# Performance work log

Measured on AMD Instinct MI355X. Metric: run time of the kernel, lower is better.

The kernel has to match this reference:

```python
import jax, jax.numpy as jnp
import numpy as np

ROT_DELTA = 1  # rotation_delta from __init__
BN_EPS = 1e-3  # keras BatchNormalization default epsilon


def conv_dirac(signal, bc_idx, bc_w, W, b):
    """Template-based intrinsic mesh conv (dirac patch operator).

    signal: [N, D]; bc_idx/bc_w: [N, Rr, A, 3]; W: [T, Rr, A, D]; b: [T].
    Returns [N, K, T] with K = A // ROT_DELTA rotations.
    """
    gathered = signal[bc_idx]  # [N, Rr, A, 3, D] irregular gather
    interp = jnp.einsum('vrai,vraid->vrad', bc_w, gathered)  # barycentric interp
    A = interp.shape[2]
    rots = np.arange(0, A, ROT_DELTA)
    # Rotating the (small) template weights is equivalent to rolling the
    # interpolated signal along the angular axis, but far cheaper.
    W_rot = jnp.stack([jnp.roll(W, int(r), axis=2) for r in rots])  # [K, T, Rr, A, D]
    return jnp.einsum('vrad,ktrad->vkt', interp, W_rot) + b  # [N, K, T]


def angular_max_pool(x):
    # Select, per vertex, the rotation whose response has maximal L2 norm.
    k = jnp.argmax(jnp.linalg.norm(x, axis=-1), axis=1)  # [N]
    return jnp.take_along_axis(x, k[:, None, None], axis=1)[:, 0]  # [N, T]


def batch_norm(x, gamma, beta):
    mu = jnp.mean(x, axis=0, keepdims=True)
    var = jnp.var(x, axis=0, keepdims=True)
    return gamma * (x - mu) * jax.lax.rsqrt(var + BN_EPS) + beta


def setup_inputs() -> dict:
    key = jax.random.key(0)
    ks = jax.random.split(key, 6)
    N, Rr, A, D, T = 80000, 5, 8, 32, 32
    signal = jax.random.normal(ks[0], (N, D), dtype=jnp.float32)
    bc_idx = jax.random.randint(ks[1], (N, Rr, A, 3), 0, N)
    bc_w = jax.random.uniform(ks[2], (N, Rr, A, 3), dtype=jnp.float32)
    bc_w = bc_w / jnp.sum(bc_w, axis=-1, keepdims=True)  # barycentric coords sum to 1
    W1 = jax.random.normal(ks[3], (T, Rr, A, D), dtype=jnp.float32) * 0.05
    W2 = jax.random.normal(ks[4], (T, Rr, A, D), dtype=jnp.float32) * 0.05
    return {
        'signal': signal, 'bc_idx': bc_idx, 'bc_w': bc_w,
        'W1': W1, 'b1': jnp.zeros((T,), jnp.float32),
        'gamma1': jnp.ones((T,), jnp.float32), 'beta1': jnp.zeros((T,), jnp.float32),
        'W2': W2, 'b2': jnp.zeros((T,), jnp.float32),
        'gamma2': jnp.ones((T,), jnp.float32), 'beta2': jnp.zeros((T,), jnp.float32),
    }


def reference(signal, bc_idx, bc_w, W1, b1, gamma1, beta1, W2, b2, gamma2, beta2):
    # Branch 1: conv -> angular max-pool -> BN -> relu
    s = conv_dirac(signal, bc_idx, bc_w, W1, b1)
    s = angular_max_pool(s)
    s = batch_norm(s, gamma1, beta1)
    s = jax.nn.relu(s)
    # Branch 2: conv -> angular max-pool -> BN
    s = conv_dirac(s, bc_idx, bc_w, W2, b2)
    s = angular_max_pool(s)
    s = batch_norm(s, gamma2, beta2)
    # Residual add (input_dim == amt_templates -> no rescale branch) + activation
    return jax.nn.relu(s + signal)
```

## Files before the change

### kernel.cpp

```cpp
#include <hip/hip_runtime.h>
#include <math.h>

#define RR 5
#define AA 8
#define DD 32
#define TT 32
#define KK 8

#define RT2 0.70710678118654752f

typedef float v2f __attribute__((ext_vector_type(2)));
typedef float v4f __attribute__((ext_vector_type(4)));

static __device__ __forceinline__ v2f pkfma(v2f a, v2f b, v2f c) {
#if __has_builtin(__builtin_elementwise_fma)
    return __builtin_elementwise_fma(a, b, c);
#else
    v2f r; r.x = fmaf(a.x, b.x, c.x); r.y = fmaf(a.y, b.y, c.y); return r;
#endif
}

__global__ void wdft_kernel(const float* __restrict__ W, float* __restrict__ Ws) {
    int idx = blockIdx.x * 256 + threadIdx.x;
    if (idx >= TT * RR * DD) return;
    int d = idx & 31;
    int tr = idx >> 5;
    int t = tr / 5;
    int r = tr - t * 5;
    float xa[8];
    #pragma unroll
    for (int a = 0; a < 8; ++a) xa[a] = W[(tr * 8 + a) * 32 + d];
    float s0 = xa[0] + xa[4], d0 = xa[0] - xa[4];
    float s1 = xa[1] + xa[5], d1 = xa[1] - xa[5];
    float s2 = xa[2] + xa[6], d2 = xa[2] - xa[6];
    float s3 = xa[3] + xa[7], d3 = xa[3] - xa[7];
    float s02 = s0 + s2, s13 = s1 + s3;
    float F0 = s02 + s13, F4 = s02 - s13;
    float R2 = s0 - s2, I2 = s3 - s1;
    float u = RT2 * (d1 - d3), v = RT2 * (d1 + d3);
    float R1 = d0 + u, R3 = d0 - u;
    float I1 = -d2 - v, I3 = d2 - v;
    float* o = &Ws[(size_t)(((r * 32 + d) * 32 + t) * 8)];
    o[0] = F0; o[1] = F4; o[2] = R1; o[3] = I1;
    o[4] = R2; o[5] = I2; o[6] = R3; o[7] = I3;
}

__global__ __launch_bounds__(256, 2)
void fused_conv_kernel(const float* __restrict__ sig,
                       const int* __restrict__ bc_idx,
                       const float* __restrict__ bc_w,
                       const float* __restrict__ Wsg,
                       const float* __restrict__ bias,
                       float* __restrict__ s_out,
                       int N) {
    __shared__ float Is[64 * 260];
    __shared__ float Wl[8 * 260];

    int tid = threadIdx.x;
    int vBase = blockIdx.x * 64;
    int lane = tid & 63;
    int wv = tid >> 6;

    int vg = lane & 7;
    int tg = lane >> 3;
    int v0L = wv * 16 + vg * 2;
    int v0 = vBase + v0L;
    int v1 = v0 + 1;

    int d2 = tid & 15;
    int g = tid >> 4;

    v2f A0[2][4], A1[2][4], A2[2][4], A3[2][4];
    #pragma unroll
    for (int vv = 0; vv < 2; ++vv)
        #pragma unroll
        for (int j = 0; j < 4; ++j) {
            A0[vv][j] = (v2f){0.f, 0.f}; A1[vv][j] = (v2f){0.f, 0.f};
            A2[vv][j] = (v2f){0.f, 0.f}; A3[vv][j] = (v2f){0.f, 0.f};
        }

    const v2f rt2 = {RT2, RT2};
    const v4f* Ws4 = (const v4f*)Wsg;

    for (int r = 0; r < RR; ++r) {
        __syncthreads();

        #pragma unroll
        for (int vv0 = 0; vv0 < 4; ++vv0) {
            int vv = g + vv0 * 16;
            int vgl = vBase + vv;
            int vgc = (vgl < N) ? vgl : (N - 1);
            int base = (vgc * 40 + r * 8) * 3;
            v2f xa[8];
            #pragma unroll
            for (int a = 0; a < 8; ++a) {
                int i0 = bc_idx[base + a * 3 + 0];
                int i1 = bc_idx[base + a * 3 + 1];
                int i2 = bc_idx[base + a * 3 + 2];
                float w0 = bc_w[base + a * 3 + 0];
                float w1 = bc_w[base + a * 3 + 1];
                float w2 = bc_w[base + a * 3 + 2];
                v2f r0 = *(const v2f*)&sig[(size_t)i0 * 32 + 2 * d2];
                v2f r1 = *(const v2f*)&sig[(size_t)i1 * 32 + 2 * d2];
                v2f r2 = *(const v2f*)&sig[(size_t)i2 * 32 + 2 * d2];
                v2f w0v = {w0, w0};
                v2f w1v = {w1, w1};
                v2f w2v = {w2, w2};
                xa[a] = pkfma(w2v, r2, pkfma(w1v, r1, w0v * r0));
            }
            v2f s0 = xa[0] + xa[4], dd0 = xa[0] - xa[4];
            v2f s1 = xa[1] + xa[5], dd1 = xa[1] - xa[5];
            v2f s2 = xa[2] + xa[6], dd2 = xa[2] - xa[6];
            v2f s3 = xa[3] + xa[7], dd3 = xa[3] - xa[7];
            v2f s02 = s0 + s2, s13 = s1 + s3;
            v2f F0 = s02 + s13, F4 = s02 - s13;
            v2f R2 = s0 - s2, I2 = s3 - s1;
            v2f u = rt2 * (dd1 - dd3), vvv = rt2 * (dd1 + dd3);
            v2f R1 = dd0 + u, R3 = dd0 - u;
            v2f I1 = -dd2 - vvv, I3 = dd2 - vvv;
            float* ob = &Is[vv * 260 + (2 * d2) * 8];
            *(v4f*)&ob[0]  = (v4f){F0.x, F4.x, R1.x, I1.x};
            *(v4f*)&ob[4]  = (v4f){R2.x, I2.x, R3.x, I3.x};
            *(v4f*)&ob[8]  = (v4f){F0.y, F4.y, R1.y, I1.y};
            *(v4f*)&ob[12] = (v4f){R2.y, I2.y, R3.y, I3.y};
        }

        for (int ws = 0; ws < 4; ++ws) {
            __syncthreads();
            {
                const v4f* src = Ws4 + (size_t)(r * 32 + ws * 8) * 64;
                int dl = tid >> 5;
                int rem = (tid * 8) & 255;
                float* dst = &Wl[dl * 260 + rem];
                v4f a = src[tid * 2];
                v4f b = src[tid * 2 + 1];
                *(v4f*)dst = a;
                *(v4f*)(dst + 4) = b;
            }
            __syncthreads();

            #pragma unroll 2
            for (int dl = 0; dl < 8; ++dl) {
                int dg = ws * 8 + dl;
                const float* ip = &Is[v0L * 260 + dg * 8];
                v4f pa0 = *(const v4f*)&ip[0];
                v4f pb0 = *(const v4f*)&ip[4];
                v4f pa1 = *(const v4f*)&ip[260];
                v4f pb1 = *(const v4f*)&ip[264];
                v2f x1_0 = pa0.zw, x1n_0 = {pa0.w, -pa0.z};
                v2f x2_0 = pb0.xy, x2n_0 = {pb0.y, -pb0.x};
                v2f x3_0 = pb0.zw, x3n_0 = {pb0.w, -pb0.z};
                v2f x1_1 = pa1.zw, x1n_1 = {pa1.w, -pa1.z};
                v2f x2_1 = pb1.xy, x2n_1 = {pb1.y, -pb1.x};
                v2f x3_1 = pb1.zw, x3n_1 = {pb1.w, -pb1.z};
                const float* wrow = &Wl[dl * 260];
                #pragma unroll
                for (int j = 0; j < 4; ++j) {
                    v4f q0 = *(const v4f*)&wrow[(tg + 8 * j) * 8];
                    v4f q1 = *(const v4f*)&wrow[(tg + 8 * j) * 8 + 4];
                    v2f w2v = {q0.z, q0.z}, w3v = {q0.w, q0.w};
                    v2f w4v = {q1.x, q1.x}, w5v = {q1.y, q1.y};
                    v2f w6v = {q1.z, q1.z}, w7v = {q1.w, q1.w};
                    A0[0][j] = pkfma(pa0.xy, q0.xy, A0[0][j]);
                    A1[0][j] = pkfma(x1_0, w2v, A1[0][j]);
                    A1[0][j] = pkfma(x1n_0, w3v, A1[0][j]);
                    A2[0][j] = pkfma(x2_0, w4v, A2[0][j]);
                    A2[0][j] = pkfma(x2n_0, w5v, A2[0][j]);
                    A3[0][j] = pkfma(x3_0, w6v, A3[0][j]);
                    A3[0][j] = pkfma(x3n_0, w7v, A3[0][j]);
                    A0[1][j] = pkfma(pa1.xy, q0.xy, A0[1][j]);
                    A1[1][j] = pkfma(x1_1, w2v, A1[1][j]);
                    A1[1][j] = pkfma(x1n_1, w3v, A1[1][j]);
                    A2[1][j] = pkfma(x2_1, w4v, A2[1][j]);
                    A2[1][j] = pkfma(x2n_1, w5v, A2[1][j]);
                    A3[1][j] = pkfma(x3_1, w6v, A3[1][j]);
                    A3[1][j] = pkfma(x3n_1, w7v, A3[1][j]);
                }
            }
        }
    }

    float bj[4];
    #pragma unroll
    for (int j = 0; j < 4; ++j) bj[j] = bias[tg + 8 * j];

    float outk[2][8][4];
    #pragma unroll
    for (int vv = 0; vv < 2; ++vv) {
        #pragma unroll
        for (int j = 0; j < 4; ++j) {
            float C0 = A0[vv][j].x, C4 = A0[vv][j].y;
            float R1 = A1[vv][j].x, I1 = A1[vv][j].y;
            float R2 = A2[vv][j].x, I2 = A2[vv][j].y;
            float R3 = A3[vv][j].x, I3 = A3[vv][j].y;
            float e = 0.125f * (C0 + C4), o = 0.125f * (C0 - C4);
            float p = 0.25f * (R1 + R3), q = 0.25f * R2, s = 0.25f * (I1 - I3);
            float a_ = 0.25f * RT2 * (R1 - R3);
            float b_ = 0.25f * RT2 * (I1 + I3);
            float c_ = 0.25f * I2;
            float bb = bj[j];
            outk[vv][0][j] = e + p + q + bb;
            outk[vv][1][j] = o + a_ - b_ - c_ + bb;
            outk[vv][2][j] = e - s - q + bb;
            outk[vv][3][j] = o - a_ - b_ + c_ + bb;
            outk[vv][4][j] = e - p + q + bb;
            outk[vv][5][j] = o - a_ + b_ - c_ + bb;
            outk[vv][6][j] = e + s - q + bb;
            outk[vv][7][j] = o + a_ + b_ + c_ + bb;
        }
    }

    #pragma unroll
    for (int vv = 0; vv < 2; ++vv) {
        float norms[8];
        #pragma unroll
        for (int k = 0; k < 8; ++k) {
            float nl = 0.f;
            #pragma unroll
            for (int j = 0; j < 4; ++j)
                nl = fmaf(outk[vv][k][j], outk[vv][k][j], nl);
            nl += __shfl_xor(nl, 8);
            nl += __shfl_xor(nl, 16);
            nl += __shfl_xor(nl, 32);
            norms[k] = nl;
        }
        float best = -1.f;
        int bk = 0;
        #pragma unroll
        for (int k = 0; k < 8; ++k) {
            float n = sqrtf(norms[k]);
            if (n > best) { best = n; bk = k; }
        }
        int vOut = (vv == 0) ? v0 : v1;
        if (vOut < N) {
            float sel[4];
            #pragma unroll
            for (int j = 0; j < 4; ++j) sel[j] = 0.f;
            #pragma unroll
            for (int k = 0; k < 8; ++k) {
                if (k == bk) {
                    #pragma unroll
                    for (int j = 0; j < 4; ++j) sel[j] = outk[vv][k][j];
                }
            }
            float* o = s_out + (size_t)vOut * 32 + tg;
            o[0]  = sel[0];
            o[8]  = sel[1];
            o[16] = sel[2];
            o[24] = sel[3];
        }
    }
}

__global__ void stats_kernel(const float* __restrict__ s,
                             double* __restrict__ sums,
                             double* __restrict__ sumsq, int n) {
    __shared__ double la[256];
    __shared__ double lb[256];
    int tid = threadIdx.x;
    int t = tid & 31;
    int row = tid >> 5;
    double a = 0.0, b = 0.0;
    for (int v = blockIdx.x * 8 + row; v < n; v += gridDim.x * 8) {
        float x = s[(size_t)v * 32 + t];
        a += (double)x;
        b += (double)x * (double)x;
    }
    la[tid] = a; lb[tid] = b;
    __syncthreads();
    for (int off = 128; off >= 32; off >>= 1) {
        if (tid < off) { la[tid] += la[tid + off]; lb[tid] += lb[tid + off]; }
        __syncthreads();
    }
    if (tid < 32) {
        atomicAdd(&sums[t], la[tid]);
        atomicAdd(&sumsq[t], lb[tid]);
    }
}

__global__ void finalize_kernel(const double* __restrict__ sums,
                                const double* __restrict__ sumsq,
                                const float* __restrict__ gamma,
                                const float* __restrict__ beta,
                                float* __restrict__ scale,
                                float* __restrict__ shift, int n) {
    int t = threadIdx.x;
    if (t < 32) {
        double mu = sums[t] / (double)n;
        double var = sumsq[t] / (double)n - mu * mu;
        double sc = (double)gamma[t] / sqrt(var + 1e-3);
        scale[t] = (float)sc;
        shift[t] = (float)((double)beta[t] - mu * sc);
    }
}

__global__ void affine_relu_kernel(const float* __restrict__ s,
                                   const float* __restrict__ scale,
                                   const float* __restrict__ shift,
                                   float* __restrict__ o, int n4) {
    int e = blockIdx.x * blockDim.x + threadIdx.x;
    if (e >= n4) return;
    int t0 = (e & 7) * 4;
    float4 x = ((const float4*)s)[e];
    float4 y;
    y.x = fmaxf(fmaf(scale[t0 + 0], x.x, shift[t0 + 0]), 0.f);
    y.y = fmaxf(fmaf(scale[t0 + 1], x.y, shift[t0 + 1]), 0.f);
    y.z = fmaxf(fmaf(scale[t0 + 2], x.z, shift[t0 + 2]), 0.f);
    y.w = fmaxf(fmaf(scale[t0 + 3], x.w, shift[t0 + 3]), 0.f);
    ((float4*)o)[e] = y;
}

__global__ void final_kernel(const float* __restrict__ s,
                             const float* __restrict__ scale,
                             const float* __restrict__ shift,
                             const float* __restrict__ sig,
                             float* __restrict__ o, int n4) {
    int e = blockIdx.x * blockDim.x + threadIdx.x;
    if (e >= n4) return;
    int t0 = (e & 7) * 4;
    float4 x = ((const float4*)s)[e];
    float4 z = ((const float4*)sig)[e];
    float4 y;
    y.x = fmaxf(fmaf(scale[t0 + 0], x.x, shift[t0 + 0]) + z.x, 0.f);
    y.y = fmaxf(fmaf(scale[t0 + 1], x.y, shift[t0 + 1]) + z.y, 0.f);
    y.z = fmaxf(fmaf(scale[t0 + 2], x.z, shift[t0 + 2]) + z.z, 0.f);
    y.w = fmaxf(fmaf(scale[t0 + 3], x.w, shift[t0 + 3]) + z.w, 0.f);
    ((float4*)o)[e] = y;
}

__global__ void zero_stats_kernel(double* __restrict__ d, float* __restrict__ f) {
    int t = threadIdx.x;
    if (t < 128) d[t] = 0.0;
    if (t < 128) f[t] = 0.f;
}

extern "C" void kernel_launch(void* const* d_in, const int* in_sizes, int n_in,
                              void* d_out, int out_size, void* d_ws, size_t ws_size,
                              hipStream_t stream) {
    const float* signal = (const float*)d_in[0];
    const int* bc_idx   = (const int*)d_in[1];
    const float* bc_w   = (const float*)d_in[2];
    const float* W1     = (const float*)d_in[3];
    const float* b1     = (const float*)d_in[4];
    const float* g1     = (const float*)d_in[5];
    const float* be1    = (const float*)d_in[6];
    const float* W2     = (const float*)d_in[7];
    const float* b2     = (const float*)d_in[8];
    const float* g2     = (const float*)d_in[9];
    const float* be2    = (const float*)d_in[10];
    float* out = (float*)d_out;

    const int N = in_sizes[0] / 32;

    char* ws = (char*)d_ws;
    double* sums1  = (double*)ws;
    double* sumsq1 = sums1 + 32;
    double* sums2  = sums1 + 64;
    double* sumsq2 = sums1 + 96;
    float* scale1 = (float*)(ws + 1024);
    float* shift1 = scale1 + 32;
    float* scale2 = scale1 + 64;
    float* shift2 = scale1 + 96;
    float* Ws1 = (float*)(ws + 4096);
    float* Ws2 = Ws1 + RR * DD * TT * 8;
    float* s1  = Ws2 + RR * DD * TT * 8;
    float* sg2 = s1 + (size_t)N * 32;
    float* s2  = sg2 + (size_t)N * 32;

    int nBlocks = (N + 63) / 64;
    int wBlocks = (TT * RR * DD + 255) / 256;

    zero_stats_kernel<<<1, 128, 0, stream>>>((double*)ws, (float*)(ws + 1024));
    wdft_kernel<<<wBlocks, 256, 0, stream>>>(W1, Ws1);
    wdft_kernel<<<wBlocks, 256, 0, stream>>>(W2, Ws2);

    fused_conv_kernel<<<nBlocks, 256, 0, stream>>>(signal, bc_idx, bc_w, Ws1, b1, s1, N);
    stats_kernel<<<64, 256, 0, stream>>>(s1, sums1, sumsq1, N);
    finalize_kernel<<<1, 32, 0, stream>>>(sums1, sumsq1, g1, be1, scale1, shift1, N);
    affine_relu_kernel<<<(N * 8 + 255) / 256, 256, 0, stream>>>(s1, scale1, shift1, sg2, N * 8);

    fused_conv_kernel<<<nBlocks, 256, 0, stream>>>(sg2, bc_idx, bc_w, Ws2, b2, s2, N);
    stats_kernel<<<64, 256, 0, stream>>>(s2, sums2, sumsq2, N);
    finalize_kernel<<<1, 32, 0, stream>>>(sums2, sumsq2, g2, be2, scale2, shift2, N);

    final_kernel<<<(N * 8 + 255) / 256, 256, 0, stream>>>(s2, scale2, shift2, signal, out, N * 8);
}
```

Baseline: 714.8 us.

## Tile conv kernel over 128 vertices with half-D staging and 4 vertices per thread

The fused conv kernel now processes 128 vertices per block. The D dimension is split into two halves of 16, and each thread gathers float4 signal chunks. Each thread accumulates 4 vertices instead of 2, so every weight value read from LDS is reused across more vertices, and the interpolation staging buffer shrinks per half. The weight DFT is also relaid out to match the new LDS layout. The costs are more accumulator registers, which may reduce occupancy, and more block syncs per radial step.

Result: slower. 2.426 ms (+239.3%).

```diff
diff --git a/kernel.cpp b/kernel.cpp
--- a/kernel.cpp
+++ b/kernel.cpp
@@ -17,6 +17,14 @@
     return __builtin_elementwise_fma(a, b, c);
 #else
     v2f r; r.x = fmaf(a.x, b.x, c.x); r.y = fmaf(a.y, b.y, c.y); return r;
+#endif
+}
+static __device__ __forceinline__ v4f pkfma4(v4f a, v4f b, v4f c) {
+#if __has_builtin(__builtin_elementwise_fma)
+    return __builtin_elementwise_fma(a, b, c);
+#else
+    v4f r; r.x = fmaf(a.x, b.x, c.x); r.y = fmaf(a.y, b.y, c.y);
+    r.z = fmaf(a.z, b.z, c.z); r.w = fmaf(a.w, b.w, c.w); return r;
 #endif
 }
 
@@ -40,9 +48,13 @@
     float u = RT2 * (d1 - d3), v = RT2 * (d1 + d3);
     float R1 = d0 + u, R3 = d0 - u;
     float I1 = -d2 - v, I3 = d2 - v;
-    float* o = &Ws[(size_t)(((r * 32 + d) * 32 + t) * 8)];
-    o[0] = F0; o[1] = F4; o[2] = R1; o[3] = I1;
-    o[4] = R2; o[5] = I2; o[6] = R3; o[7] = I3;
+    int h = d >> 4;
+    int sub = (d >> 3) & 1;
+    int dl = d & 7;
+    float* o0 = &Ws[(size_t)(((r * 2 + h) * 2 + sub) * 2 + 0) * 1024 + dl * 128 + t * 4];
+    float* o1 = o0 + 1024;
+    o0[0] = F0; o0[1] = F4; o0[2] = R1; o0[3] = I1;
+    o1[0] = R2; o1[1] = I2; o1[2] = R3; o1[3] = I3;
 }
 
 __global__ __launch_bounds__(256, 2)
@@ -53,128 +65,130 @@
                        const float* __restrict__ bias,
                        float* __restrict__ s_out,
                        int N) {
-    __shared__ float Is[64 * 260];
-    __shared__ float Wl[8 * 260];
+    __shared__ float Is[128 * 132];
+    __shared__ float Wl[2048];
 
     int tid = threadIdx.x;
-    int vBase = blockIdx.x * 64;
+    int vBase = blockIdx.x * 128;
     int lane = tid & 63;
     int wv = tid >> 6;
 
     int vg = lane & 7;
     int tg = lane >> 3;
-    int v0L = wv * 16 + vg * 2;
-    int v0 = vBase + v0L;
-    int v1 = v0 + 1;
-
-    int d2 = tid & 15;
-    int g = tid >> 4;
-
-    v2f A0[2][4], A1[2][4], A2[2][4], A3[2][4];
+
+    int d4 = tid & 3;
+    int g = tid >> 2;
+
+    v2f A0[4][4], A1[4][4], A2[4][4], A3[4][4];
     #pragma unroll
-    for (int vv = 0; vv < 2; ++vv)
+    for (int vv = 0; vv < 4; ++vv)
         #pragma unroll
         for (int j = 0; j < 4; ++j) {
             A0[vv][j] = (v2f){0.f, 0.f}; A1[vv][j] = (v2f){0.f, 0.f};
             A2[vv][j] = (v2f){0.f, 0.f}; A3[vv][j] = (v2f){0.f, 0.f};
         }
 
-    const v2f rt2 = {RT2, RT2};
-    const v4f* Ws4 = (const v4f*)Wsg;
-
     for (int r = 0; r < RR; ++r) {
-        __syncthreads();
-
-        #pragma unroll
-        for (int vv0 = 0; vv0 < 4; ++vv0) {
-            int vv = g + vv0 * 16;
-            int vgl = vBase + vv;
-            int vgc = (vgl < N) ? vgl : (N - 1);
-            int base = (vgc * 40 + r * 8) * 3;
-            v2f xa[8];
-            #pragma unroll
-            for (int a = 0; a < 8; ++a) {
-                int i0 = bc_idx[base + a * 3 + 0];
-                int i1 = bc_idx[base + a * 3 + 1];
-                int i2 = bc_idx[base + a * 3 + 2];
-                float w0 = bc_w[base + a * 3 + 0];
-                float w1 = bc_w[base + a * 3 + 1];
-                float w2 = bc_w[base + a * 3 + 2];
-                v2f r0 = *(const v2f*)&sig[(size_t)i0 * 32 + 2 * d2];
-                v2f r1 = *(const v2f*)&sig[(size_t)i1 * 32 + 2 * d2];
-                v2f r2 = *(const v2f*)&sig[(size_t)i2 * 32 + 2 * d2];
-                v2f w0v = {w0, w0};
-                v2f w1v = {w1, w1};
-                v2f w2v = {w2, w2};
-                xa[a] = pkfma(w2v, r2, pkfma(w1v, r1, w0v * r0));
+        for (int h = 0; h < 2; ++h) {
+            __syncthreads();
+
+            {
+                const float* src = Wsg + (size_t)((r * 2 + h) * 2 + 0) * 2048 + tid * 8;
+                v4f a = *(const v4f*)src;
+                v4f b = *(const v4f*)(src + 4);
+                *(v4f*)&Wl[tid * 8] = a;
+                *(v4f*)&Wl[tid * 8 + 4] = b;
             }
-            v2f s0 = xa[0] + xa[4], dd0 = xa[0] - xa[4];
-            v2f s1 = xa[1] + xa[5], dd1 = xa[1] - xa[5];
-            v2f s2 = xa[2] + xa[6], dd2 = xa[2] - xa[6];
-            v2f s3 = xa[3] + xa[7], dd3 = xa[3] - xa[7];
-            v2f s02 = s0 + s2, s13 = s1 + s3;
-            v2f F0 = s02 + s13, F4 = s02 - s13;
-            v2f R2 = s0 - s2, I2 = s3 - s1;
-            v2f u = rt2 * (dd1 - dd3), vvv = rt2 * (dd1 + dd3);
-            v2f R1 = dd0 + u, R3 = dd0 - u;
-            v2f I1 = -dd2 - vvv, I3 = dd2 - vvv;
-            float* ob = &Is[vv * 260 + (2 * d2) * 8];
-            *(v4f*)&ob[0]  = (v4f){F0.x, F4.x, R1.x, I1.x};
-            *(v4f*)&ob[4]  = (v4f){R2.x, I2.x, R3.x, I3.x};
-            *(v4f*)&ob[8]  = (v4f){F0.y, F4.y, R1.y, I1.y};
-            *(v4f*)&ob[12] = (v4f){R2.y, I2.y, R3.y, I3.y};
-        }
-
-        for (int ws = 0; ws < 4; ++ws) {
-            __syncthreads();
-            {
-                const v4f* src = Ws4 + (size_t)(r * 32 + ws * 8) * 64;
-                int dl = tid >> 5;
-                int rem = (tid * 8) & 255;
-                float* dst = &Wl[dl * 260 + rem];
-                v4f a = src[tid * 2];
-                v4f b = src[tid * 2 + 1];
-                *(v4f*)dst = a;
-                *(v4f*)(dst + 4) = b;
+
+            #pragma unroll
+            for (int pass = 0; pass < 2; ++pass) {
+                int vv = g + 64 * pass;
+                int vgl = vBase + vv;
+                int vgc = (vgl < N) ? vgl : (N - 1);
+                int base = (vgc * 40 + r * 8) * 3;
+                v4f xa[8];
+                #pragma unroll
+                for (int a = 0; a < 8; ++a) {
+                    int i0 = bc_idx[base + a * 3 + 0];
+                    int i1 = bc_idx[base + a * 3 + 1];
+                    int i2 = bc_idx[base + a * 3 + 2];
+                    float w0 = bc_w[base + a * 3 + 0];
+                    float w1 = bc_w[base + a * 3 + 1];
+                    float w2 = bc_w[base + a * 3 + 2];
+                    v4f r0 = *(const v4f*)&sig[(size_t)i0 * 32 + h * 16 + d4 * 4];
+                    v4f r1 = *(const v4f*)&sig[(size_t)i1 * 32 + h * 16 + d4 * 4];
+                    v4f r2 = *(const v4f*)&sig[(size_t)i2 * 32 + h * 16 + d4 * 4];
+                    v4f w0v = {w0, w0, w0, w0};
+                    v4f w1v = {w1, w1, w1, w1};
+                    v4f w2v = {w2, w2, w2, w2};
+                    xa[a] = pkfma4(w2v, r2, pkfma4(w1v, r1, w0v * r0));
+                }
+                v4f s0 = xa[0] + xa[4], dd0 = xa[0] - xa[4];
+                v4f s1 = xa[1] + xa[5], dd1 = xa[1] - xa[5];
+                v4f s2 = xa[2] + xa[6], dd2 = xa[2] - xa[6];
+                v4f s3 = xa[3] + xa[7], dd3 = xa[3] - xa[7];
+                v4f s02 = s0 + s2, s13 = s1 + s3;
+                v4f F0 = s02 + s13, F4 = s02 - s13;
+                v4f R2 = s0 - s2, I2 = s3 - s1;
+                v4f rt2v = {RT2, RT2, RT2, RT2};
+                v4f u = rt2v * (dd1 - dd3), vvv = rt2v * (dd1 + dd3);
+                v4f R1 = dd0 + u, R3 = dd0 - u;
+                v4f I1 = -dd2 - vvv, I3 = dd2 - vvv;
+                float* ob = &Is[vv * 132];
+                #pragma unroll
+                for (int c = 0; c < 4; ++c) {
+                    int dloc = 4 * d4 + c;
+                    *(v4f*)&ob[dloc * 4]      = (v4f){F0[c], F4[c], R1[c], I1[c]};
+                    *(v4f*)&ob[64 + dloc * 4] = (v4f){R2[c], I2[c], R3[c], I3[c]};
+                }
             }
-            __syncthreads();
-
-            #pragma unroll 2
-            for (int dl = 0; dl < 8; ++dl) {
-                int dg = ws * 8 + dl;
-                const float* ip = &Is[v0L * 260 + dg * 8];
-                v4f pa0 = *(const v4f*)&ip[0];
-                v4f pb0 = *(const v4f*)&ip[4];
-                v4f pa1 = *(const v4f*)&ip[260];
-                v4f pb1 = *(const v4f*)&ip[264];
-                v2f x1_0 = pa0.zw, x1n_0 = {pa0.w, -pa0.z};
-                v2f x2_0 = pb0.xy, x2n_0 = {pb0.y, -pb0.x};
-                v2f x3_0 = pb0.zw, x3n_0 = {pb0.w, -pb0.z};
-                v2f x1_1 = pa1.zw, x1n_1 = {pa1.w, -pa1.z};
-                v2f x2_1 = pb1.xy, x2n_1 = {pb1.y, -pb1.x};
-                v2f x3_1 = pb1.zw, x3n_1 = {pb1.w, -pb1.z};
-                const float* wrow = &Wl[dl * 260];
-                #pragma unroll
-                for (int j = 0; j < 4; ++j) {
-                    v4f q0 = *(const v4f*)&wrow[(tg + 8 * j) * 8];
-                    v4f q1 = *(const v4f*)&wrow[(tg + 8 * j) * 8 + 4];
-                    v2f w2v = {q0.z, q0.z}, w3v = {q0.w, q0.w};
-                    v2f w4v = {q1.x, q1.x}, w5v = {q1.y, q1.y};
-                    v2f w6v = {q1.z, q1.z}, w7v = {q1.w, q1.w};
-                    A0[0][j] = pkfma(pa0.xy, q0.xy, A0[0][j]);
-                    A1[0][j] = pkfma(x1_0, w2v, A1[0][j]);
-                    A1[0][j] = pkfma(x1n_0, w3v, A1[0][j]);
-                    A2[0][j] = pkfma(x2_0, w4v, A2[0][j]);
-                    A2[0][j] = pkfma(x2n_0, w5v, A2[0][j]);
-                    A3[0][j] = pkfma(x3_0, w6v, A3[0][j]);
-                    A3[0][j] = pkfma(x3n_0, w7v, A3[0][j]);
-                    A0[1][j] = pkfma(pa1.xy, q0.xy, A0[1][j]);
-                    A1[1][j] = pkfma(x1_1, w2v, A1[1][j]);
-                    A1[1][j] = pkfma(x1n_1, w3v, A1[1][j]);
-                    A2[1][j] = pkfma(x2_1, w4v, A2[1][j]);
-                    A2[1][j] = pkfma(x2n_1, w5v, A2[1][j]);
-                    A3[1][j] = pkfma(x3_1, w6v, A3[1][j]);
-                    A3[1][j] = pkfma(x3n_1, w7v, A3[1][j]);
+
+            #pragma unroll
+            for (int sub = 0; sub < 2; ++sub) {
+                if (sub == 1) {
+                    __syncthreads();
+                    const float* src = Wsg + (size_t)((r * 2 + h) * 2 + 1) * 2048 + tid * 8;
+                    v4f a = *(const v4f*)src;
+                    v4f b = *(const v4f*)(src + 4);
+                    *(v4f*)&Wl[tid * 8] = a;
+                    *(v4f*)&Wl[tid * 8 + 4] = b;
+                }
+                __syncthreads();
+
+                #pragma unroll 2
+                for (int dl = 0; dl < 8; ++dl) {
+                    int dloc = sub * 8 + dl;
+                    v4f p0[4], p1[4];
+                    #pragma unroll
+                    for (int vv = 0; vv < 4; ++vv) {
+                        int vrow = wv * 32 + vg + vv * 8;
+                        p0[vv] = *(const v4f*)&Is[vrow * 132 + dloc * 4];
+                        p1[vv] = *(const v4f*)&Is[vrow * 132 + 64 + dloc * 4];
+                    }
+                    #pragma unroll
+                    for (int j = 0; j < 4; ++j) {
+                        v4f q0 = *(const v4f*)&Wl[dl * 128 + (tg + 8 * j) * 4];
+                        v4f q1 = *(const v4f*)&Wl[1024 + dl * 128 + (tg + 8 * j) * 4];
+                        v2f w2v = {q0.z, q0.z}, w3v = {q0.w, q0.w};
+                        v2f w4v = {q1.x, q1.x}, w5v = {q1.y, q1.y};
+                        v2f w6v = {q1.z, q1.z}, w7v = {q1.w, q1.w};
+                        #pragma unroll
+                        for (int vv = 0; vv < 4; ++vv) {
+                            v2f x1 = p0[vv].zw;
+                            v2f x1n = {p0[vv].w, -p0[vv].z};
+                            v2f x2 = p1[vv].xy;
+                            v2f x2n = {p1[vv].y, -p1[vv].x};
+                            v2f x3 = p1[vv].zw;
+                            v2f x3n = {p1[vv].w, -p1[vv].z};
+                            A0[vv][j] = pkfma(p0[vv].xy, q0.xy, A0[vv][j]);
+                            A1[vv][j] = pkfma(x1, w2v, A1[vv][j]);
+                            A1[vv][j] = pkfma(x1n, w3v, A1[vv][j]);
+                            A2[vv][j] = pkfma(x2, w4v, A2[vv][j]);
+                            A2[vv][j] = pkfma(x2n, w5v, A2[vv][j]);
+                            A3[vv][j] = pkfma(x3, w6v, A3[vv][j]);
+                            A3[vv][j] = pkfma(x3n, w7v, A3[vv][j]);
+                        }
+                    }
                 }
             }
         }
@@ -184,9 +198,9 @@
     #pragma unroll
     for (int j = 0; j < 4; ++j) bj[j] = bias[tg + 8 * j];
 
-    float outk[2][8][4];
     #pragma unroll
-    for (int vv = 0; vv < 2; ++vv) {
+    for (int vv = 0; vv < 4; ++vv) {
+        float outk[8][4];
         #pragma unroll
         for (int j = 0; j < 4; ++j) {
             float C0 = A0[vv][j].x, C4 = A0[vv][j].y;
@@ -199,26 +213,22 @@
             float b_ = 0.25f * RT2 * (I1 + I3);
             float c_ = 0.25f * I2;
             float bb = bj[j];
-            outk[vv][0][j] = e + p + q + bb;
-            outk[vv][1][j] = o + a_ - b_ - c_ + bb;
-            outk[vv][2][j] = e - s - q + bb;
-            outk[vv][3][j] = o - a_ - b_ + c_ + bb;
-            outk[vv][4][j] = e - p + q + bb;
-            outk[vv][5][j] = o - a_ + b_ - c_ + bb;
-            outk[vv][6][j] = e + s - q + bb;
-            outk[vv][7][j] = o + a_ + b_ + c_ + bb;
-        }
-    }
-
-    #pragma unroll
-    for (int vv = 0; vv < 2; ++vv) {
+            outk[0][j] = e + p + q + bb;
+            outk[1][j] = o + a_ - b_ - c_ + bb;
+            outk[2][j] = e - s - q + bb;
+            outk[3][j] = o - a_ - b_ + c_ + bb;
+            outk[4][j] = e - p + q + bb;
+            outk[5][j] = o - a_ + b_ - c_ + bb;
+            outk[6][j] = e + s - q + bb;
+            outk[7][j] = o + a_ + b_ + c_ + bb;
+        }
         float norms[8];
         #pragma unroll
         for (int k = 0; k < 8; ++k) {
             float nl = 0.f;
             #pragma unroll
             for (int j = 0; j < 4; ++j)
-                nl = fmaf(outk[vv][k][j], outk[vv][k][j], nl);
+                nl = fmaf(outk[k][j], outk[k][j], nl);
             nl += __shfl_xor(nl, 8);
             nl += __shfl_xor(nl, 16);
             nl += __shfl_xor(nl, 32);
@@ -231,7 +241,7 @@
             float n = sqrtf(norms[k]);
             if (n > best) { best = n; bk = k; }
         }
-        int vOut = (vv == 0) ? v0 : v1;
+        int vOut = vBase + wv * 32 + vg + vv * 8;
         if (vOut < N) {
             float sel[4];
             #pragma unroll
@@ -240,7 +250,7 @@
             for (int k = 0; k < 8; ++k) {
                 if (k == bk) {
                     #pragma unroll
-                    for (int j = 0; j < 4; ++j) sel[j] = outk[vv][k][j];
+                    for (int j = 0; j < 4; ++j) sel[j] = outk[k][j];
                 }
             }
             float* o = s_out + (size_t)vOut * 32 + tg;
@@ -367,7 +377,7 @@
     float* sg2 = s1 + (size_t)N * 32;
     float* s2  = sg2 + (size_t)N * 32;
 
-    int nBlocks = (N + 63) / 64;
+    int nBlocks = (N + 127) / 128;
     int wBlocks = (TT * RR * DD + 255) / 256;
 
     zero_stats_kernel<<<1, 128, 0, stream>>>((double*)ws, (float*)(ws + 1024));
```

## Fuse BN1+ReLU into second conv gather and halve shared-memory tiles for occupancy

Applied to the files above, without the earlier changes.

Removes the standalone affine+ReLU pass by applying BN1 scale/shift and ReLU to gathered neighbor values inside the second conv kernel, which is templated on an AFFINE flag. The conv now processes the feature dimension in two halves of 16, with a new weight layout and a smaller shared-memory footprint. This allows launch bounds of 3 blocks per SM. Each gathered value is now re-transformed per use (three neighbors per angle), and the interpolation stage syncs more often, trading extra ALU work and barriers for one fewer full-tensor read/write and higher occupancy.

After: 808.7 us. 13.1% more time.

```diff
diff --git a/kernel.cpp b/kernel.cpp
--- a/kernel.cpp
+++ b/kernel.cpp
@@ -40,21 +40,27 @@
     float u = RT2 * (d1 - d3), v = RT2 * (d1 + d3);
     float R1 = d0 + u, R3 = d0 - u;
     float I1 = -d2 - v, I3 = d2 - v;
-    float* o = &Ws[(size_t)(((r * 32 + d) * 32 + t) * 8)];
-    o[0] = F0; o[1] = F4; o[2] = R1; o[3] = I1;
-    o[4] = R2; o[5] = I2; o[6] = R3; o[7] = I3;
-}
-
-__global__ __launch_bounds__(256, 2)
+    int h = d >> 4;
+    int dl = d & 15;
+    float* o0 = &Ws[(size_t)(r * 2 + h) * 4096 + dl * 128 + t * 4];
+    float* o1 = o0 + 2048;
+    o0[0] = F0; o0[1] = F4; o0[2] = R1; o0[3] = I1;
+    o1[0] = R2; o1[1] = I2; o1[2] = R3; o1[3] = I3;
+}
+
+template <bool AFFINE>
+__global__ __launch_bounds__(256, 3)
 void fused_conv_kernel(const float* __restrict__ sig,
                        const int* __restrict__ bc_idx,
                        const float* __restrict__ bc_w,
                        const float* __restrict__ Wsg,
                        const float* __restrict__ bias,
                        float* __restrict__ s_out,
+                       const float* __restrict__ scaleIn,
+                       const float* __restrict__ shiftIn,
                        int N) {
-    __shared__ float Is[64 * 260];
-    __shared__ float Wl[8 * 260];
+    __shared__ float Is[64 * 132];
+    __shared__ float Wl[4096];
 
     int tid = threadIdx.x;
     int vBase = blockIdx.x * 64;
@@ -63,12 +69,18 @@
 
     int vg = lane & 7;
     int tg = lane >> 3;
-    int v0L = wv * 16 + vg * 2;
-    int v0 = vBase + v0L;
-    int v1 = v0 + 1;
-
-    int d2 = tid & 15;
-    int g = tid >> 4;
+
+    int d2 = tid & 7;
+    int g = tid >> 3;
+
+    v2f scH[2], shH[2];
+    if (AFFINE) {
+        #pragma unroll
+        for (int h = 0; h < 2; ++h) {
+            scH[h] = *(const v2f*)&scaleIn[h * 16 + 2 * d2];
+            shH[h] = *(const v2f*)&shiftIn[h * 16 + 2 * d2];
+        }
+    }
 
     v2f A0[2][4], A1[2][4], A2[2][4], A3[2][4];
     #pragma unroll
@@ -80,101 +92,105 @@
         }
 
     const v2f rt2 = {RT2, RT2};
-    const v4f* Ws4 = (const v4f*)Wsg;
+    int vrow0 = (wv * 16 + vg) * 132;
+    int vrow1 = vrow0 + 8 * 132;
 
     for (int r = 0; r < RR; ++r) {
-        __syncthreads();
-
-        #pragma unroll
-        for (int vv0 = 0; vv0 < 4; ++vv0) {
-            int vv = g + vv0 * 16;
-            int vgl = vBase + vv;
-            int vgc = (vgl < N) ? vgl : (N - 1);
-            int base = (vgc * 40 + r * 8) * 3;
-            v2f xa[8];
+        #pragma unroll
+        for (int h = 0; h < 2; ++h) {
+            __syncthreads();
+
+            {
+                const v4f* src = (const v4f*)(Wsg + (size_t)(r * 2 + h) * 4096);
+                #pragma unroll
+                for (int k = 0; k < 4; ++k) {
+                    v4f val = src[k * 256 + tid];
+                    *(v4f*)&Wl[k * 1024 + tid * 4] = val;
+                }
+            }
+
             #pragma unroll
-            for (int a = 0; a < 8; ++a) {
-                int i0 = bc_idx[base + a * 3 + 0];
-                int i1 = bc_idx[base + a * 3 + 1];
-                int i2 = bc_idx[base + a * 3 + 2];
-                float w0 = bc_w[base + a * 3 + 0];
-                float w1 = bc_w[base + a * 3 + 1];
-                float w2 = bc_w[base + a * 3 + 2];
-                v2f r0 = *(const v2f*)&sig[(size_t)i0 * 32 + 2 * d2];
-                v2f r1 = *(const v2f*)&sig[(size_t)i1 * 32 + 2 * d2];
-                v2f r2 = *(const v2f*)&sig[(size_t)i2 * 32 + 2 * d2];
-                v2f w0v = {w0, w0};
-                v2f w1v = {w1, w1};
-                v2f w2v = {w2, w2};
-                xa[a] = pkfma(w2v, r2, pkfma(w1v, r1, w0v * r0));
-            }
-            v2f s0 = xa[0] + xa[4], dd0 = xa[0] - xa[4];
-            v2f s1 = xa[1] + xa[5], dd1 = xa[1] - xa[5];
-            v2f s2 = xa[2] + xa[6], dd2 = xa[2] - xa[6];
-            v2f s3 = xa[3] + xa[7], dd3 = xa[3] - xa[7];
-            v2f s02 = s0 + s2, s13 = s1 + s3;
-            v2f F0 = s02 + s13, F4 = s02 - s13;
-            v2f R2 = s0 - s2, I2 = s3 - s1;
-            v2f u = rt2 * (dd1 - dd3), vvv = rt2 * (dd1 + dd3);
-            v2f R1 = dd0 + u, R3 = dd0 - u;
-            v2f I1 = -dd2 - vvv, I3 = dd2 - vvv;
-            float* ob = &Is[vv * 260 + (2 * d2) * 8];
-            *(v4f*)&ob[0]  = (v4f){F0.x, F4.x, R1.x, I1.x};
-            *(v4f*)&ob[4]  = (v4f){R2.x, I2.x, R3.x, I3.x};
-            *(v4f*)&ob[8]  = (v4f){F0.y, F4.y, R1.y, I1.y};
-            *(v4f*)&ob[12] = (v4f){R2.y, I2.y, R3.y, I3.y};
-        }
-
-        for (int ws = 0; ws < 4; ++ws) {
-            __syncthreads();
-            {
-                const v4f* src = Ws4 + (size_t)(r * 32 + ws * 8) * 64;
-                int dl = tid >> 5;
-                int rem = (tid * 8) & 255;
-                float* dst = &Wl[dl * 260 + rem];
-                v4f a = src[tid * 2];
-                v4f b = src[tid * 2 + 1];
-                *(v4f*)dst = a;
-                *(v4f*)(dst + 4) = b;
+            for (int pass = 0; pass < 2; ++pass) {
+                int vv = g + 32 * pass;
+                int vgl = vBase + vv;
+                int vgc = (vgl < N) ? vgl : (N - 1);
+                int base = (vgc * 40 + r * 8) * 3;
+                v2f xa[8];
+                #pragma unroll
+                for (int a = 0; a < 8; ++a) {
+                    int i0 = bc_idx[base + a * 3 + 0];
+                    int i1 = bc_idx[base + a * 3 + 1];
+                    int i2 = bc_idx[base + a * 3 + 2];
+                    float w0 = bc_w[base + a * 3 + 0];
+                    float w1 = bc_w[base + a * 3 + 1];
+                    float w2 = bc_w[base + a * 3 + 2];
+                    v2f r0 = *(const v2f*)&sig[(size_t)i0 * 32 + h * 16 + 2 * d2];
+                    v2f r1 = *(const v2f*)&sig[(size_t)i1 * 32 + h * 16 + 2 * d2];
+                    v2f r2 = *(const v2f*)&sig[(size_t)i2 * 32 + h * 16 + 2 * d2];
+                    if (AFFINE) {
+                        r0.x = fmaxf(fmaf(scH[h].x, r0.x, shH[h].x), 0.f);
+                        r0.y = fmaxf(fmaf(scH[h].y, r0.y, shH[h].y), 0.f);
+                        r1.x = fmaxf(fmaf(scH[h].x, r1.x, shH[h].x), 0.f);
+                        r1.y = fmaxf(fmaf(scH[h].y, r1.y, shH[h].y), 0.f);
+                        r2.x = fmaxf(fmaf(scH[h].x, r2.x, shH[h].x), 0.f);
+                        r2.y = fmaxf(fmaf(scH[h].y, r2.y, shH[h].y), 0.f);
+                    }
+                    v2f w0v = {w0, w0};
+                    v2f w1v = {w1, w1};
+                    v2f w2v = {w2, w2};
+                    xa[a] = pkfma(w2v, r2, pkfma(w1v, r1, w0v * r0));
+                }
+                v2f s0 = xa[0] + xa[4], dd0 = xa[0] - xa[4];
+                v2f s1 = xa[1] + xa[5], dd1 = xa[1] - xa[5];
+                v2f s2 = xa[2] + xa[6], dd2 = xa[2] - xa[6];
+                v2f s3 = xa[3] + xa[7], dd3 = xa[3] - xa[7];
+                v2f s02 = s0 + s2, s13 = s1 + s3;
+                v2f F0 = s02 + s13, F4 = s02 - s13;
+                v2f R2 = s0 - s2, I2 = s3 - s1;
+                v2f u = rt2 * (dd1 - dd3), vvv = rt2 * (dd1 + dd3);
+                v2f R1 = dd0 + u, R3 = dd0 - u;
+                v2f I1 = -dd2 - vvv, I3 = dd2 - vvv;
+                float* ob = &Is[vv * 132 + d2 * 16];
+                *(v4f*)&ob[0]  = (v4f){F0.x, F4.x, R1.x, I1.x};
+                *(v4f*)&ob[4]  = (v4f){R2.x, I2.x, R3.x, I3.x};
+                *(v4f*)&ob[8]  = (v4f){F0.y, F4.y, R1.y, I1.y};
+                *(v4f*)&ob[12] = (v4f){R2.y, I2.y, R3.y, I3.y};
             }
             __syncthreads();
 
             #pragma unroll 2
-            for (int dl = 0; dl < 8; ++dl) {
-                int dg = ws * 8 + dl;
-                const float* ip = &Is[v0L * 260 + dg * 8];
-                v4f pa0 = *(const v4f*)&ip[0];
-                v4f pb0 = *(const v4f*)&ip[4];
-                v4f pa1 = *(const v4f*)&ip[260];
-                v4f pb1 = *(const v4f*)&ip[264];
-                v2f x1_0 = pa0.zw, x1n_0 = {pa0.w, -pa0.z};
-                v2f x2_0 = pb0.xy, x2n_0 = {pb0.y, -pb0.x};
-                v2f x3_0 = pb0.zw, x3n_0 = {pb0.w, -pb0.z};
-                v2f x1_1 = pa1.zw, x1n_1 = {pa1.w, -pa1.z};
-                v2f x2_1 = pb1.xy, x2n_1 = {pb1.y, -pb1.x};
-                v2f x3_1 = pb1.zw, x3n_1 = {pb1.w, -pb1.z};
-                const float* wrow = &Wl[dl * 260];
+            for (int dl = 0; dl < 16; ++dl) {
+                v4f p0a = *(const v4f*)&Is[vrow0 + dl * 8];
+                v4f p1a = *(const v4f*)&Is[vrow0 + dl * 8 + 4];
+                v4f p0b = *(const v4f*)&Is[vrow1 + dl * 8];
+                v4f p1b = *(const v4f*)&Is[vrow1 + dl * 8 + 4];
+                v2f x1a = p0a.zw, x1na = {p0a.w, -p0a.z};
+                v2f x2a = p1a.xy, x2na = {p1a.y, -p1a.x};
+                v2f x3a = p1a.zw, x3na = {p1a.w, -p1a.z};
+                v2f x1b = p0b.zw, x1nb = {p0b.w, -p0b.z};
+                v2f x2b = p1b.xy, x2nb = {p1b.y, -p1b.x};
+                v2f x3b = p1b.zw, x3nb = {p1b.w, -p1b.z};
                 #pragma unroll
                 for (int j = 0; j < 4; ++j) {
-                    v4f q0 = *(const v4f*)&wrow[(tg + 8 * j) * 8];
-                    v4f q1 = *(const v4f*)&wrow[(tg + 8 * j) * 8 + 4];
+                    v4f q0 = *(const v4f*)&Wl[dl * 128 + (tg + 8 * j) * 4];
+                    v4f q1 = *(const v4f*)&Wl[2048 + dl * 128 + (tg + 8 * j) * 4];
                     v2f w2v = {q0.z, q0.z}, w3v = {q0.w, q0.w};
                     v2f w4v = {q1.x, q1.x}, w5v = {q1.y, q1.y};
                     v2f w6v = {q1.z, q1.z}, w7v = {q1.w, q1.w};
-                    A0[0][j] = pkfma(pa0.xy, q0.xy, A0[0][j]);
-                    A1[0][j] = pkfma(x1_0, w2v, A1[0][j]);
-                    A1[0][j] = pkfma(x1n_0, w3v, A1[0][j]);
-                    A2[0][j] = pkfma(x2_0, w4v, A2[0][j]);
-                    A2[0][j] = pkfma(x2n_0, w5v, A2[0][j]);
-                    A3[0][j] = pkfma(x3_0, w6v, A3[0][j]);
-                    A3[0][j] = pkfma(x3n_0, w7v, A3[0][j]);
-                    A0[1][j] = pkfma(pa1.xy, q0.xy, A0[1][j]);
-                    A1[1][j] = pkfma(x1_1, w2v, A1[1][j]);
-                    A1[1][j] = pkfma(x1n_1, w3v, A1[1][j]);
-                    A2[1][j] = pkfma(x2_1, w4v, A2[1][j]);
-                    A2[1][j] = pkfma(x2n_1, w5v, A2[1][j]);
-                    A3[1][j] = pkfma(x3_1, w6v, A3[1][j]);
-                    A3[1][j] = pkfma(x3n_1, w7v, A3[1][j]);
+                    A0[0][j] = pkfma(p0a.xy, q0.xy, A0[0][j]);
+                    A1[0][j] = pkfma(x1a, w2v, A1[0][j]);
+                    A1[0][j] = pkfma(x1na, w3v, A1[0][j]);
+                    A2[0][j] = pkfma(x2a, w4v, A2[0][j]);
+                    A2[0][j] = pkfma(x2na, w5v, A2[0][j]);
+                    A3[0][j] = pkfma(x3a, w6v, A3[0][j]);
+                    A3[0][j] = pkfma(x3na, w7v, A3[0][j]);
+                    A0[1][j] = pkfma(p0b.xy, q0.xy, A0[1][j]);
+                    A1[1][j] = pkfma(x1b, w2v, A1[1][j]);
+                    A1[1][j] = pkfma(x1nb, w3v, A1[1][j]);
+                    A2[1][j] = pkfma(x2b, w4v, A2[1][j]);
+                    A2[1][j] = pkfma(x2nb, w5v, A2[1][j]);
+                    A3[1][j] = pkfma(x3b, w6v, A3[1][j]);
+                    A3[1][j] = pkfma(x3nb, w7v, A3[1][j]);
                 }
             }
         }
@@ -184,9 +200,9 @@
     #pragma unroll
     for (int j = 0; j < 4; ++j) bj[j] = bias[tg + 8 * j];
 
-    float outk[2][8][4];
     #pragma unroll
     for (int vv = 0; vv < 2; ++vv) {
+        float outk[8][4];
         #pragma unroll
         for (int j = 0; j < 4; ++j) {
             float C0 = A0[vv][j].x, C4 = A0[vv][j].y;
@@ -199,26 +215,22 @@
             float b_ = 0.25f * RT2 * (I1 + I3);
             float c_ = 0.25f * I2;
             float bb = bj[j];
-            outk[vv][0][j] = e + p + q + bb;
-            outk[vv][1][j] = o + a_ - b_ - c_ + bb;
-            outk[vv][2][j] = e - s - q + bb;
-            outk[vv][3][j] = o - a_ - b_ + c_ + bb;
-            outk[vv][4][j] = e - p + q + bb;
-            outk[vv][5][j] = o - a_ + b_ - c_ + bb;
-            outk[vv][6][j] = e + s - q + bb;
-            outk[vv][7][j] = o + a_ + b_ + c_ + bb;
-        }
-    }
-
-    #pragma unroll
-    for (int vv = 0; vv < 2; ++vv) {
+            outk[0][j] = e + p + q + bb;
+            outk[1][j] = o + a_ - b_ - c_ + bb;
+            outk[2][j] = e - s - q + bb;
+            outk[3][j] = o - a_ - b_ + c_ + bb;
+            outk[4][j] = e - p + q + bb;
+            outk[5][j] = o - a_ + b_ - c_ + bb;
+            outk[6][j] = e + s - q + bb;
+            outk[7][j] = o + a_ + b_ + c_ + bb;
+        }
         float norms[8];
         #pragma unroll
         for (int k = 0; k < 8; ++k) {
             float nl = 0.f;
             #pragma unroll
             for (int j = 0; j < 4; ++j)
-                nl = fmaf(outk[vv][k][j], outk[vv][k][j], nl);
+                nl = fmaf(outk[k][j], outk[k][j], nl);
             nl += __shfl_xor(nl, 8);
             nl += __shfl_xor(nl, 16);
             nl += __shfl_xor(nl, 32);
@@ -231,7 +243,7 @@
             float n = sqrtf(norms[k]);
             if (n > best) { best = n; bk = k; }
         }
-        int vOut = (vv == 0) ? v0 : v1;
+        int vOut = vBase + wv * 16 + vg + 8 * vv;
         if (vOut < N) {
             float sel[4];
             #pragma unroll
@@ -240,7 +252,7 @@
             for (int k = 0; k < 8; ++k) {
                 if (k == bk) {
                     #pragma unroll
-                    for (int j = 0; j < 4; ++j) sel[j] = outk[vv][k][j];
+                    for (int j = 0; j < 4; ++j) sel[j] = outk[k][j];
                 }
             }
             float* o = s_out + (size_t)vOut * 32 + tg;
@@ -292,22 +304,6 @@
         scale[t] = (float)sc;
         shift[t] = (float)((double)beta[t] - mu * sc);
     }
-}
-
-__global__ void affine_relu_kernel(const float* __restrict__ s,
-                                   const float* __restrict__ scale,
-                                   const float* __restrict__ shift,
-                                   float* __restrict__ o, int n4) {
-    int e = blockIdx.x * blockDim.x + threadIdx.x;
-    if (e >= n4) return;
-    int t0 = (e & 7) * 4;
-    float4 x = ((const float4*)s)[e];
-    float4 y;
-    y.x = fmaxf(fmaf(scale[t0 + 0], x.x, shift[t0 + 0]), 0.f);
-    y.y = fmaxf(fmaf(scale[t0 + 1], x.y, shift[t0 + 1]), 0.f);
-    y.z = fmaxf(fmaf(scale[t0 + 2], x.z, shift[t0 + 2]), 0.f);
-    y.w = fmaxf(fmaf(scale[t0 + 3], x.w, shift[t0 + 3]), 0.f);
-    ((float4*)o)[e] = y;
 }
 
 __global__ void final_kernel(const float* __restrict__ s,
@@ -364,8 +360,7 @@
     float* Ws1 = (float*)(ws + 4096);
     float* Ws2 = Ws1 + RR * DD * TT * 8;
     float* s1  = Ws2 + RR * DD * TT * 8;
-    float* sg2 = s1 + (size_t)N * 32;
-    float* s2  = sg2 + (size_t)N * 32;
+    float* s2  = s1 + (size_t)N * 32;
 
     int nBlocks = (N + 63) / 64;
     int wBlocks = (TT * RR * DD + 255) / 256;
@@ -374,12 +369,13 @@
     wdft_kernel<<<wBlocks, 256, 0, stream>>>(W1, Ws1);
     wdft_kernel<<<wBlocks, 256, 0, stream>>>(W2, Ws2);
 
-    fused_conv_kernel<<<nBlocks, 256, 0, stream>>>(signal, bc_idx, bc_w, Ws1, b1, s1, N);
+    fused_conv_kernel<false><<<nBlocks, 256, 0, stream>>>(
+        signal, bc_idx, bc_w, Ws1, b1, s1, nullptr, nullptr, N);
     stats_kernel<<<64, 256, 0, stream>>>(s1, sums1, sumsq1, N);
     finalize_kernel<<<1, 32, 0, stream>>>(sums1, sumsq1, g1, be1, scale1, shift1, N);
-    affine_relu_kernel<<<(N * 8 + 255) / 256, 256, 0, stream>>>(s1, scale1, shift1, sg2, N * 8);
-
-    fused_conv_kernel<<<nBlocks, 256, 0, stream>>>(sg2, bc_idx, bc_w, Ws2, b2, s2, N);
+
+    fused_conv_kernel<true><<<nBlocks, 256, 0, stream>>>(
+        s1, bc_idx, bc_w, Ws2, b2, s2, scale1, shift1, N);
     stats_kernel<<<64, 256, 0, stream>>>(s2, sums2, sumsq2, N);
     finalize_kernel<<<1, 32, 0, stream>>>(sums2, sumsq2, g2, be2, scale2, shift2, N);
 
```
